# Performance work log

Hardware: AMD Instinct MI355X
Metric: run time of the kernel (lower is better)

Reference implementation:

```python
import jax, jax.numpy as jnp
import numpy as np
from jax import lax

B, T, DEPTH = 512, 32, 512
RNN, NCC = 512, 128
D_IN = DEPTH * (T * DEPTH // T // DEPTH) * 1 + NCC  # slice_len=1 -> 512 + 128 = 640


def setup_inputs() -> dict:
    key = jax.random.key(0)
    ks = jax.random.split(key, 7)
    s = 0.05  # tf.random_normal_initializer default stddev
    return {
        "f_pool": jax.random.normal(ks[0], (B, T, DEPTH), jnp.float32),
        "ground_truth": jax.random.normal(ks[1], (B, T, NCC), jnp.float32),
        "kernel": jax.random.normal(ks[2], (DEPTH + NCC, 4 * RNN), jnp.float32) * s,
        "rec_kernel": jax.random.normal(ks[3], (RNN, 4 * RNN), jnp.float32) * s,
        "bias": jax.random.normal(ks[4], (4 * RNN,), jnp.float32) * s,
        "softmax_w": jax.random.normal(ks[5], (RNN, NCC), jnp.float32) * s,
        "softmax_b": jax.random.normal(ks[6], (NCC,), jnp.float32) * s,
    }


def reference(f_pool, ground_truth, kernel, rec_kernel, bias, softmax_w, softmax_b):
    b, features_num, depth = f_pool.shape
    seq_length = ground_truth.shape[1]
    ncc = softmax_b.shape[0]
    rnn = rec_kernel.shape[0]
    slice_len = features_num // seq_length  # == 1 here
    gt_t = jnp.transpose(ground_truth, (1, 0, 2))  # [T, B, C] for scan

    def step(carry, inp):
        h, c, prev = carry
        t, gt_row = inp
        # image feature slice at char index t -> [B, slice_len*depth]
        feat = lax.dynamic_slice_in_dim(f_pool, t, slice_len, axis=1)
        feat = feat.reshape(b, slice_len * depth)
        x = jnp.concatenate([feat, prev], axis=1)
        z = x @ kernel + h @ rec_kernel + bias  # [B, 4*rnn]
        i, f, g, o = jnp.split(z, 4, axis=1)    # keras LSTMCell gate order
        c2 = jax.nn.sigmoid(f) * c + jax.nn.sigmoid(i) * jnp.tanh(g)
        h2 = jax.nn.sigmoid(o) * jnp.tanh(c2)
        logits = h2 @ softmax_w + softmax_b
        onehot = jax.nn.one_hot(jnp.argmax(logits, axis=1), ncc, dtype=f_pool.dtype)
        # teacher forcing: prev_output = ground_truth[:, t, :]
        return (h2, c2, gt_row), onehot

    h0 = jnp.zeros((b, rnn), f_pool.dtype)
    c0 = jnp.zeros((b, rnn), f_pool.dtype)
    prev0 = jnp.zeros((b, ncc), f_pool.dtype)
    (h, c, _), outs = lax.scan(step, (h0, c0, prev0), (jnp.arange(seq_length), gt_t))
    sequence_output = jnp.transpose(outs, (1, 0, 2))  # [B, T, C]
    return (sequence_output, h, c)
```

## Files before the change

kernel.cpp:

```cpp
#include <hip/hip_runtime.h>
#include <math.h>

typedef float  f32x4  __attribute__((ext_vector_type(4)));
typedef short  short8v __attribute__((ext_vector_type(8)));
typedef unsigned short ushort8v __attribute__((ext_vector_type(8)));
typedef unsigned short ushort4v __attribute__((ext_vector_type(4)));

#define KP_PRE 3840
#define KP_HS  1536

#define WAITV(N) asm volatile("s_waitcnt vmcnt(" #N ")" ::: "memory")
#define SBAR()   asm volatile("s_barrier" ::: "memory")

__device__ unsigned short g_Xb[16384][3840];
__device__ unsigned short g_Wb[2048][3840];
__device__ unsigned short g_Rb[2048][1536];
__device__ unsigned short g_hs[2][512][1536];
__device__ float g_pre[16384][2048];
__device__ float g_hf[2][512 * 512];
__device__ float g_swT[128][512];
__device__ float g_bperm[2048];
__device__ float g_plv[2][512 * 8];
__device__ int   g_pli[2][512 * 8];
__device__ unsigned g_xcnt[128];
__device__ unsigned g_xrel[128];

__global__ void init_counters()
{
    int t = threadIdx.x;
    if (t < 8) { g_xcnt[t * 16] = 0u; g_xrel[t * 16] = 0u; }
}

__device__ __forceinline__ unsigned short f2bf(float f) {
    unsigned u = __float_as_uint(f);
    return (unsigned short)((u + 0x7fffu + ((u >> 16) & 1u)) >> 16);
}
__device__ __forceinline__ float bf2f(unsigned short s) {
    return __uint_as_float(((unsigned)s) << 16);
}
__device__ __forceinline__ float sigf(float x) { return 1.f / (1.f + expf(-x)); }

__device__ __forceinline__ void split3(float v, unsigned short& s0,
                                       unsigned short& s1, unsigned short& s2) {
    s0 = f2bf(v); float f0 = bf2f(s0);
    s1 = f2bf(v - f0); float f1 = bf2f(s1);
    s2 = f2bf(v - f0 - f1);
}

__device__ __constant__ int c_ipt[6] = {0, 0, 1, 0, 1, 2};
__device__ __constant__ int c_jpt[6] = {0, 1, 0, 2, 1, 0};

__device__ __forceinline__ void gl16(const unsigned short* g, unsigned short* l) {
    __builtin_amdgcn_global_load_lds((const __attribute__((address_space(1))) void*)g,
                                     (__attribute__((address_space(3))) void*)l, 16, 0, 0);
}

__device__ __forceinline__ short8v fragld(const unsigned short* sh, int row, int uw) {
    return *(const short8v*)(sh + row * 64 + ((uw ^ (row & 7)) << 3));
}

template<int AUNITS, int BUNITS>
__device__ __forceinline__ void stage_chunk(const unsigned short* Ag, int pitchA,
                                            const unsigned short* Bg, int pitchB,
                                            int kb, unsigned short* slot, int tid)
{
#pragma unroll
    for (int v = 0; v < AUNITS / 256; ++v) {
        int e = v * 256 + tid;
        gl16(Ag + (size_t)(e >> 3) * pitchA + kb * 64 + (e & 7) * 8, slot + e * 8);
    }
#pragma unroll
    for (int v = 0; v < BUNITS / 256; ++v) {
        int e = v * 256 + tid;
        gl16(Bg + (size_t)(e >> 3) * pitchB + kb * 64 + (e & 7) * 8,
             slot + AUNITS * 8 + e * 8);
    }
}

__device__ __forceinline__ void stageA3(const unsigned short* Ag, int kr,
                                        unsigned short* buf, int tid)
{
#pragma unroll
    for (int s = 0; s < 3; ++s)
#pragma unroll
        for (int v = 0; v < 2; ++v) {
            int e = v * 256 + tid;
            gl16(Ag + (size_t)(e >> 3) * KP_HS + (s * 8 + kr) * 64 + (e & 7) * 8,
                 buf + s * 4096 + e * 8);
        }
}
__device__ __forceinline__ void stageB3(const unsigned short* Bg, int kr,
                                        unsigned short* buf, int tid)
{
#pragma unroll
    for (int s = 0; s < 3; ++s)
#pragma unroll
        for (int v = 0; v < 2; ++v) {
            int e = v * 256 + tid;
            gl16(Bg + (size_t)(e >> 3) * KP_HS + (s * 8 + kr) * 64 + (e & 7) * 8,
                 buf + 12288 + s * 4096 + e * 8);
        }
}
__device__ __forceinline__ void stage6(const unsigned short* Ag,
                                       const unsigned short* Bg,
                                       int kr, unsigned short* buf, int tid)
{
    stageA3(Ag, kr, buf, tid);
    stageB3(Bg, kr, buf, tid);
}

__global__ __launch_bounds__(256) void build_Xb(const float* __restrict__ fp,
                                                const float* __restrict__ gt)
{
    const int tid = threadIdx.x;
    const int m  = blockIdx.x * 16 + (tid >> 4);
    const int k8 = (blockIdx.y * 16 + (tid & 15)) * 8;
    const int t = m >> 9, b = m & 511;
    float x[8];
    if (k8 < 512) {
        float4 v0 = *(const float4*)(fp + ((size_t)(b * 32 + t)) * 512 + k8);
        float4 v1 = *(const float4*)(fp + ((size_t)(b * 32 + t)) * 512 + k8 + 4);
        x[0]=v0.x; x[1]=v0.y; x[2]=v0.z; x[3]=v0.w;
        x[4]=v1.x; x[5]=v1.y; x[6]=v1.z; x[7]=v1.w;
    } else if (t > 0) {
        float4 v0 = *(const float4*)(gt + ((size_t)(b * 32 + t - 1)) * 128 + (k8 - 512));
        float4 v1 = *(const float4*)(gt + ((size_t)(b * 32 + t - 1)) * 128 + (k8 - 512) + 4);
        x[0]=v0.x; x[1]=v0.y; x[2]=v0.z; x[3]=v0.w;
        x[4]=v1.x; x[5]=v1.y; x[6]=v1.z; x[7]=v1.w;
    } else {
#pragma unroll
        for (int j = 0; j < 8; ++j) x[j] = 0.f;
    }
    unsigned short s0[8], s1[8], s2[8];
#pragma unroll
    for (int j = 0; j < 8; ++j) split3(x[j], s0[j], s1[j], s2[j]);
    const int u = (k8 >> 3) & 7;
    const int base = (k8 & ~63) + (((u ^ (m & 7))) << 3);
#pragma unroll
    for (int p = 0; p < 6; ++p) {
        ushort8v v;
#pragma unroll
        for (int j = 0; j < 8; ++j)
            v[j] = (c_ipt[p] == 0) ? s0[j] : ((c_ipt[p] == 1) ? s1[j] : s2[j]);
        *(ushort8v*)&g_Xb[m][p * 640 + base] = v;
    }
}

__global__ __launch_bounds__(256) void build_Wb(const float* __restrict__ Wk)
{
    const int tid = threadIdx.x;
    const int np = blockIdx.x * 16 + (tid >> 4);
    const int k8 = (blockIdx.y * 16 + (tid & 15)) * 8;
    const int n = (np & 3) * 512 + (np >> 2);
    float x[8];
#pragma unroll
    for (int j = 0; j < 8; ++j) x[j] = Wk[(size_t)(k8 + j) * 2048 + n];
    unsigned short s0[8], s1[8], s2[8];
#pragma unroll
    for (int j = 0; j < 8; ++j) split3(x[j], s0[j], s1[j], s2[j]);
    const int u = (k8 >> 3) & 7;
    const int base = (k8 & ~63) + (((u ^ (np & 7))) << 3);
#pragma unroll
    for (int p = 0; p < 6; ++p) {
        ushort8v v;
#pragma unroll
        for (int j = 0; j < 8; ++j)
            v[j] = (c_jpt[p] == 0) ? s0[j] : ((c_jpt[p] == 1) ? s1[j] : s2[j]);
        *(ushort8v*)&g_Wb[np][p * 640 + base] = v;
    }
}

__global__ __launch_bounds__(256) void build_Rb(const float* __restrict__ Rk)
{
    const int tid = threadIdx.x;
    const int np = blockIdx.x * 16 + (tid >> 4);
    const int k8 = (blockIdx.y * 16 + (tid & 15)) * 8;
    const int n = (np & 3) * 512 + (np >> 2);
    float x[8];
#pragma unroll
    for (int j = 0; j < 8; ++j) x[j] = Rk[(size_t)(k8 + j) * 2048 + n];
    unsigned short s0[8], s1[8], s2[8];
#pragma unroll
    for (int j = 0; j < 8; ++j) split3(x[j], s0[j], s1[j], s2[j]);
    const int u = (k8 >> 3) & 7;
    const int base = (k8 & ~63) + (((u ^ (np & 7))) << 3);
    ushort8v v0, v1, v2;
#pragma unroll
    for (int j = 0; j < 8; ++j) { v0[j] = s0[j]; v1[j] = s1[j]; v2[j] = s2[j]; }
    *(ushort8v*)&g_Rb[np][0 * 512 + base] = v0;
    *(ushort8v*)&g_Rb[np][1 * 512 + base] = v1;
    *(ushort8v*)&g_Rb[np][2 * 512 + base] = v2;
}

__global__ __launch_bounds__(256) void build_misc(const float* __restrict__ sw,
                                                  const float* __restrict__ bias)
{
    int id = blockIdx.x * 256 + threadIdx.x;
    if (id < 128 * 512) {
        int c = id >> 9, r = id & 511;
        g_swT[c][r] = sw[(size_t)r * 128 + c];
    } else if (id < 128 * 512 + 2048) {
        int np = id - 128 * 512;
        g_bperm[np] = bias[(np & 3) * 512 + (np >> 2)];
    }
}

__global__ __launch_bounds__(256, 1) void pre_mfma()
{
    __shared__ __align__(16) char smem[98304];
    const int tid = threadIdx.x, lane = tid & 63, wave = tid >> 6;
    const int n0 = blockIdx.x * 64, m0 = blockIdx.y * 128;
    const int wr = wave >> 1, wc = wave & 1, l15 = lane & 15, ql = lane >> 4;
    unsigned short* ring = (unsigned short*)smem;
    const unsigned short* Ag = &g_Xb[m0][0];
    const unsigned short* Bg = &g_Wb[n0][0];

    f32x4 acc[4][2];
#pragma unroll
    for (int a = 0; a < 4; ++a)
#pragma unroll
        for (int b = 0; b < 2; ++b) acc[a][b] = (f32x4){0.f, 0.f, 0.f, 0.f};

    stage_chunk<1024, 512>(Ag, KP_PRE, Bg, KP_PRE, 0, ring + 0 * 12288, tid);
    stage_chunk<1024, 512>(Ag, KP_PRE, Bg, KP_PRE, 1, ring + 1 * 12288, tid);
    stage_chunk<1024, 512>(Ag, KP_PRE, Bg, KP_PRE, 2, ring + 2 * 12288, tid);
    for (int c = 0; c < 60; ++c) {
        if (c <= 57)      WAITV(12);
        else if (c == 58) WAITV(6);
        else              WAITV(0);
        SBAR();
        const unsigned short* Ac = ring + (c & 3) * 12288;
        const unsigned short* Bc = Ac + 8192;
#pragma unroll
        for (int sub = 0; sub < 2; ++sub) {
            const int uw = sub * 4 + ql;
            short8v af[4], bfr[2];
#pragma unroll
            for (int fa = 0; fa < 4; ++fa)
                af[fa] = fragld(Ac, wr * 64 + fa * 16 + l15, uw);
#pragma unroll
            for (int fb = 0; fb < 2; ++fb)
                bfr[fb] = fragld(Bc, wc * 32 + fb * 16 + l15, uw);
#pragma unroll
            for (int fa = 0; fa < 4; ++fa)
#pragma unroll
                for (int fb = 0; fb < 2; ++fb)
                    acc[fa][fb] = __builtin_amdgcn_mfma_f32_16x16x32_bf16(
                        af[fa], bfr[fb], acc[fa][fb], 0, 0, 0);
        }
        if (c + 3 < 60)
            stage_chunk<1024, 512>(Ag, KP_PRE, Bg, KP_PRE, c + 3,
                                   ring + ((c + 3) & 3) * 12288, tid);
    }
#pragma unroll
    for (int fa = 0; fa < 4; ++fa)
#pragma unroll
        for (int fb = 0; fb < 2; ++fb) {
            const int np = n0 + wc * 32 + fb * 16 + l15;
            const float bv = g_bperm[np];
#pragma unroll
            for (int q = 0; q < 4; ++q) {
                const int m = m0 + wr * 64 + fa * 16 + ql * 4 + q;
                g_pre[m][np] = acc[fa][fb][q] + bv;
            }
        }
}

__global__ __launch_bounds__(256, 1) void charnn_rec(
    const float* __restrict__ sb,
    float* __restrict__ seq, float* __restrict__ out_h, float* __restrict__ out_c)
{
    __shared__ __align__(16) char smem[147456];
    float (*zbuf)[68] = (float (*)[68])smem;
    unsigned short* ring = (unsigned short*)smem;

    const int bi = blockIdx.x, tid = threadIdx.x;
    const int lane = tid & 63, wave = tid >> 6;
    const int x  = bi & 7, jj = bi >> 3;
    const int Mg = x;
    const int Ng = jj;
    const int m0 = Mg * 64, n0 = Ng * 64;
    const int wr = wave >> 1, wc = wave & 1, l15 = lane & 15, ql = lane >> 4;

    const int m_e = tid >> 2;
    const int rb4 = (tid & 3) * 4;
    const int mg = m0 + m_e;
    float cst[4] = {0.f, 0.f, 0.f, 0.f};

    const int rgrp = Mg * 4 + (jj & 3);
    const int cg   = jj >> 2;
    const int arow = Mg * 64 + jj * 2;
    const bool xleader = (jj == 0);

    constexpr int ipt[6] = {0, 0, 1, 0, 1, 2};
    constexpr int jpt[6] = {0, 1, 0, 2, 1, 0};

    const unsigned short* Bg = &g_Rb[n0][0];

    f32x4 pq0, pq1, pq2, pq3;
    {
        const float* prow = &g_pre[0 * 512 + mg][n0];
        pq0 = *(const f32x4*)(prow + rb4 * 4);
        pq1 = *(const f32x4*)(prow + rb4 * 4 + 4);
        pq2 = *(const f32x4*)(prow + rb4 * 4 + 8);
        pq3 = *(const f32x4*)(prow + rb4 * 4 + 12);
    }

    for (int ph = 0; ph < 34; ++ph) {
        const int t = ph;
        const bool do_z = (ph >= 1 && ph <= 31);

        const unsigned short* Ag = nullptr;
        if (do_z) {
            Ag = &g_hs[(t + 1) & 1][m0][0];
            stageA3(Ag, 0, ring + 0 * 24576, tid);
            stageA3(Ag, 1, ring + 1 * 24576, tid);
            stageA3(Ag, 2, ring + 2 * 24576, tid);
        }

        if (ph >= 1 && ph <= 32) {
            const int tl = ph - 1;
            const int row = rgrp * 16 + (tid >> 4);
            const int col = cg * 16 + (tid & 15);
            const float* hrow = &g_hf[tl & 1][(size_t)row * 512];
            const float* wcol = &g_swT[col][0];
            float s0 = sb[col], s1 = 0.f, s2 = 0.f, s3 = 0.f;
#pragma unroll 8
            for (int k = 0; k < 512; k += 4) {
                float4 hv = *(const float4*)(hrow + k);
                float4 wv = *(const float4*)(wcol + k);
                s0 = fmaf(hv.x, wv.x, s0); s1 = fmaf(hv.y, wv.y, s1);
                s2 = fmaf(hv.z, wv.z, s2); s3 = fmaf(hv.w, wv.w, s3);
            }
            float bv = (s0 + s1) + (s2 + s3); int bidx = col;
#pragma unroll
            for (int m = 1; m < 16; m <<= 1) {
                float ov = __shfl_xor(bv, m, 64);
                int   oi = __shfl_xor(bidx, m, 64);
                if (ov > bv || (ov == bv && oi < bidx)) { bv = ov; bidx = oi; }
            }
            if ((tid & 15) == 0) {
                g_plv[tl & 1][row * 8 + cg] = bv;
                g_pli[tl & 1][row * 8 + cg] = bidx;
            }
        }

        if (ph >= 2 && wave < 2) {
            const int t2 = ph - 2;
            const int row = arow + wave;
            float v; int idx;
            if (lane < 8) {
                v   = g_plv[t2 & 1][row * 8 + lane];
                idx = g_pli[t2 & 1][row * 8 + lane];
            } else { v = -INFINITY; idx = 0x7fffffff; }
#pragma unroll
            for (int m = 1; m < 8; m <<= 1) {
                float ov = __shfl_xor(v, m, 64);
                int   oi = __shfl_xor(idx, m, 64);
                if (ov > v || (ov == v && oi < idx)) { v = ov; idx = oi; }
            }
            int win = __shfl(idx, 0, 64);
            if (lane < 32) {
                int c4 = lane * 4;
                float4 o;
                o.x = (c4 + 0 == win) ? 1.f : 0.f;
                o.y = (c4 + 1 == win) ? 1.f : 0.f;
                o.z = (c4 + 2 == win) ? 1.f : 0.f;
                o.w = (c4 + 3 == win) ? 1.f : 0.f;
                *(float4*)(seq + ((size_t)row * 32 + t2) * 128 + c4) = o;
            }
        }

        if (ph <= 31) {
            if (do_z) {
                f32x4 acc[2][2];
#pragma unroll
                for (int a = 0; a < 2; ++a)
#pragma unroll
                    for (int b = 0; b < 2; ++b) acc[a][b] = (f32x4){0.f, 0.f, 0.f, 0.f};
#pragma unroll
                for (int kr = 0; kr < 8; ++kr) {
                    if (kr >= 1 && kr <= 5)
                        stage6(Ag, Bg, kr + 2, ring + ((kr + 2) % 3) * 24576, tid);
                    if      (kr == 0) WAITV(12);
                    else if (kr == 1) WAITV(18);
                    else if (kr == 2) WAITV(24);
                    else if (kr == 3) WAITV(24);
                    else if (kr == 4) WAITV(24);
                    else if (kr == 5) WAITV(24);
                    else if (kr == 6) WAITV(12);
                    else              WAITV(0);
                    SBAR();
                    const unsigned short* Ab = ring + (kr % 3) * 24576;
                    const unsigned short* Bb = Ab + 12288;
#pragma unroll
                    for (int sub = 0; sub < 2; ++sub) {
                        const int uw = sub * 4 + ql;
                        short8v a0[2], a1[2], a2[2], b0[2], b1[2], b2[2];
                        a0[0] = fragld(Ab + 0 * 4096, wr * 32 + l15, uw);
                        a0[1] = fragld(Ab + 0 * 4096, wr * 32 + 16 + l15, uw);
                        a1[0] = fragld(Ab + 1 * 4096, wr * 32 + l15, uw);
                        a1[1] = fragld(Ab + 1 * 4096, wr * 32 + 16 + l15, uw);
                        a2[0] = fragld(Ab + 2 * 4096, wr * 32 + l15, uw);
                        a2[1] = fragld(Ab + 2 * 4096, wr * 32 + 16 + l15, uw);
                        b0[0] = fragld(Bb + 0 * 4096, wc * 32 + l15, uw);
                        b0[1] = fragld(Bb + 0 * 4096, wc * 32 + 16 + l15, uw);
                        b1[0] = fragld(Bb + 1 * 4096, wc * 32 + l15, uw);
                        b1[1] = fragld(Bb + 1 * 4096, wc * 32 + 16 + l15, uw);
                        b2[0] = fragld(Bb + 2 * 4096, wc * 32 + l15, uw);
                        b2[1] = fragld(Bb + 2 * 4096, wc * 32 + 16 + l15, uw);
#pragma unroll
                        for (int p = 0; p < 6; ++p) {
                            const short8v* A2 = (ipt[p] == 0) ? a0 :
                                                ((ipt[p] == 1) ? a1 : a2);
                            const short8v* B2 = (jpt[p] == 0) ? b0 :
                                                ((jpt[p] == 1) ? b1 : b2);
                            acc[0][0] = __builtin_amdgcn_mfma_f32_16x16x32_bf16(
                                A2[0], B2[0], acc[0][0], 0, 0, 0);
                            acc[0][1] = __builtin_amdgcn_mfma_f32_16x16x32_bf16(
                                A2[0], B2[1], acc[0][1], 0, 0, 0);
                            acc[1][0] = __builtin_amdgcn_mfma_f32_16x16x32_bf16(
                                A2[1], B2[0], acc[1][0], 0, 0, 0);
                            acc[1][1] = __builtin_amdgcn_mfma_f32_16x16x32_bf16(
                                A2[1], B2[1], acc[1][1], 0, 0, 0);
                        }
                    }
                }
                __syncthreads();
#pragma unroll
                for (int fa = 0; fa < 2; ++fa)
#pragma unroll
                    for (int fb = 0; fb < 2; ++fb)
#pragma unroll
                        for (int q2 = 0; q2 < 4; ++q2)
                            zbuf[wr * 32 + fa * 16 + ql * 4 + q2]
                                [wc * 32 + fb * 16 + l15] = acc[fa][fb][q2];
            }
            __syncthreads();

            unsigned short hs0[4], hs1[4], hs2[4];
            float hv4[4];
#pragma unroll
            for (int i = 0; i < 4; ++i) {
                const int rl = rb4 + i;
                float zi, zf, zg, zo;
                if (t > 0) {
                    float4 zq = *(const float4*)&zbuf[m_e][rl * 4];
                    zi = zq.x; zf = zq.y; zg = zq.z; zo = zq.w;
                } else { zi = zf = zg = zo = 0.f; }
                f32x4 pq = (i == 0) ? pq0 : ((i == 1) ? pq1 : ((i == 2) ? pq2 : pq3));
                zi += pq[0]; zf += pq[1]; zg += pq[2]; zo += pq[3];
                float c2 = sigf(zf) * cst[i] + sigf(zi) * tanhf(zg);
                float h2 = sigf(zo) * tanhf(c2);
                cst[i] = c2;
                hv4[i] = h2;
                split3(h2, hs0[i], hs1[i], hs2[i]);
            }
            const int r0g = Ng * 16 + rb4;
            *(float4*)&g_hf[t & 1][(size_t)mg * 512 + r0g] =
                make_float4(hv4[0], hv4[1], hv4[2], hv4[3]);
            if (t == 31) {
                *(float4*)&out_h[(size_t)mg * 512 + r0g] =
                    make_float4(hv4[0], hv4[1], hv4[2], hv4[3]);
                *(float4*)&out_c[(size_t)mg * 512 + r0g] =
                    make_float4(cst[0], cst[1], cst[2], cst[3]);
            }
            const int su = ((r0g >> 3) & 7) ^ (mg & 7);
            const int abase = (r0g & ~63) + (su << 3) + (r0g & 7);
#pragma unroll
            for (int i = 0; i < 3; ++i) {
                ushort4v v;
#pragma unroll
                for (int j = 0; j < 4; ++j)
                    v[j] = (i == 0) ? hs0[j] : ((i == 1) ? hs1[j] : hs2[j]);
                *(ushort4v*)&g_hs[t & 1][mg][i * 512 + abase] = v;
            }
        }

        if (ph < 33) {
            __syncthreads();

            if (ph <= 30) {
                stageB3(Bg, 0, ring + 0 * 24576, tid);
                stageB3(Bg, 1, ring + 1 * 24576, tid);
                stageB3(Bg, 2, ring + 2 * 24576, tid);
                const float* prow = &g_pre[(ph + 1) * 512 + mg][n0];
                pq0 = *(const f32x4*)(prow + rb4 * 4);
                pq1 = *(const f32x4*)(prow + rb4 * 4 + 4);
                pq2 = *(const f32x4*)(prow + rb4 * 4 + 8);
                pq3 = *(const f32x4*)(prow + rb4 * 4 + 12);
            }

            if (tid == 0) {
                __hip_atomic_fetch_add(&g_xcnt[x * 16], 1u,
                                       __ATOMIC_RELAXED, __HIP_MEMORY_SCOPE_AGENT);
                if (xleader) {
                    const unsigned xt = 32u * (unsigned)(ph + 1);
                    while (__hip_atomic_load(&g_xcnt[x * 16], __ATOMIC_RELAXED,
                                             __HIP_MEMORY_SCOPE_AGENT) < xt)
                        __builtin_amdgcn_s_sleep(2);
                    __hip_atomic_store(&g_xrel[x * 16], (unsigned)(ph + 1),
                                       __ATOMIC_RELAXED, __HIP_MEMORY_SCOPE_AGENT);
                }
                while (__hip_atomic_load(&g_xrel[x * 16], __ATOMIC_RELAXED,
                                         __HIP_MEMORY_SCOPE_AGENT) < (unsigned)(ph + 1))
                    __builtin_amdgcn_s_sleep(2);
                __builtin_amdgcn_fence(__ATOMIC_ACQUIRE, "agent");
            }
            __syncthreads();
        }
    }
}

extern "C" void kernel_launch(void* const* d_in, const int* in_sizes, int n_in,
                              void* d_out, int out_size, void* d_ws, size_t ws_size,
                              hipStream_t stream)
{
    const float* fp   = (const float*)d_in[0];
    const float* gt   = (const float*)d_in[1];
    const float* Wk   = (const float*)d_in[2];
    const float* Rk   = (const float*)d_in[3];
    const float* bias = (const float*)d_in[4];
    const float* sw   = (const float*)d_in[5];
    const float* sb   = (const float*)d_in[6];
    float* seq   = (float*)d_out;
    float* out_h = seq + (size_t)512 * 32 * 128;
    float* out_c = out_h + (size_t)512 * 512;

    hipLaunchKernelGGL(init_counters, dim3(1), dim3(64), 0, stream);
    hipLaunchKernelGGL(build_Xb, dim3(1024, 5), dim3(256), 0, stream, fp, gt);
    hipLaunchKernelGGL(build_Wb, dim3(128, 5), dim3(256), 0, stream, Wk);
    hipLaunchKernelGGL(build_Rb, dim3(128, 4), dim3(256), 0, stream, Rk);
    hipLaunchKernelGGL(build_misc, dim3(264), dim3(256), 0, stream, sw, bias);
    hipLaunchKernelGGL(pre_mfma, dim3(32, 128), dim3(256), 0, stream);
    hipLaunchKernelGGL(charnn_rec, dim3(256), dim3(256), 0, stream,
                       sb, seq, out_h, out_c);
}
```

Measured before the change: 1.711 ms.

## Double recurrent kernel block to 512 threads, halving per-wave MFMA and gate work

The persistent recurrent LSTM kernel now launches 512 threads per block instead of 256. Each of 8 waves computes a 32x16 output tile instead of 32x32, each thread handles two gate rows instead of four, and each thread issues half as many staging loads, with the vmcnt waits adjusted to match. The aim is to shorten the serial per-step critical path by spreading MFMA, LDS fragment loads and the gate epilogue over more waves. In exchange, the A fragments are loaded twice as often across waves and the block-wide barriers cost more with more waves.

```diff
diff --git a/kernel.cpp b/kernel.cpp
--- a/kernel.cpp
+++ b/kernel.cpp
@@ -4,7 +4,7 @@
 typedef float  f32x4  __attribute__((ext_vector_type(4)));
 typedef short  short8v __attribute__((ext_vector_type(8)));
 typedef unsigned short ushort8v __attribute__((ext_vector_type(8)));
-typedef unsigned short ushort4v __attribute__((ext_vector_type(4)));
+typedef unsigned short ushort2v __attribute__((ext_vector_type(2)));
 
 #define KP_PRE 3840
 #define KP_HS  1536
@@ -77,36 +77,32 @@
     }
 }
 
-__device__ __forceinline__ void stageA3(const unsigned short* Ag, int kr,
-                                        unsigned short* buf, int tid)
-{
-#pragma unroll
-    for (int s = 0; s < 3; ++s)
-#pragma unroll
-        for (int v = 0; v < 2; ++v) {
-            int e = v * 256 + tid;
-            gl16(Ag + (size_t)(e >> 3) * KP_HS + (s * 8 + kr) * 64 + (e & 7) * 8,
-                 buf + s * 4096 + e * 8);
-        }
-}
-__device__ __forceinline__ void stageB3(const unsigned short* Bg, int kr,
-                                        unsigned short* buf, int tid)
-{
-#pragma unroll
-    for (int s = 0; s < 3; ++s)
-#pragma unroll
-        for (int v = 0; v < 2; ++v) {
-            int e = v * 256 + tid;
-            gl16(Bg + (size_t)(e >> 3) * KP_HS + (s * 8 + kr) * 64 + (e & 7) * 8,
-                 buf + 12288 + s * 4096 + e * 8);
-        }
-}
-__device__ __forceinline__ void stage6(const unsigned short* Ag,
-                                       const unsigned short* Bg,
-                                       int kr, unsigned short* buf, int tid)
-{
-    stageA3(Ag, kr, buf, tid);
-    stageB3(Bg, kr, buf, tid);
+__device__ __forceinline__ void stageA3w(const unsigned short* Ag, int kr,
+                                         unsigned short* buf, int tid)
+{
+#pragma unroll
+    for (int s = 0; s < 3; ++s) {
+        int e = tid;
+        gl16(Ag + (size_t)(e >> 3) * KP_HS + (s * 8 + kr) * 64 + (e & 7) * 8,
+             buf + s * 4096 + e * 8);
+    }
+}
+__device__ __forceinline__ void stageB3w(const unsigned short* Bg, int kr,
+                                         unsigned short* buf, int tid)
+{
+#pragma unroll
+    for (int s = 0; s < 3; ++s) {
+        int e = tid;
+        gl16(Bg + (size_t)(e >> 3) * KP_HS + (s * 8 + kr) * 64 + (e & 7) * 8,
+             buf + 12288 + s * 4096 + e * 8);
+    }
+}
+__device__ __forceinline__ void stage6w(const unsigned short* Ag,
+                                        const unsigned short* Bg,
+                                        int kr, unsigned short* buf, int tid)
+{
+    stageA3w(Ag, kr, buf, tid);
+    stageB3w(Bg, kr, buf, tid);
 }
 
 __global__ __launch_bounds__(256) void build_Xb(const float* __restrict__ fp,
@@ -266,7 +262,7 @@
         }
 }
 
-__global__ __launch_bounds__(256, 1) void charnn_rec(
+__global__ __launch_bounds__(512, 1) void charnn_rec(
     const float* __restrict__ sb,
     float* __restrict__ seq, float* __restrict__ out_h, float* __restrict__ out_c)
 {
@@ -280,12 +276,12 @@
     const int Mg = x;
     const int Ng = jj;
     const int m0 = Mg * 64, n0 = Ng * 64;
-    const int wr = wave >> 1, wc = wave & 1, l15 = lane & 15, ql = lane >> 4;
-
-    const int m_e = tid >> 2;
-    const int rb4 = (tid & 3) * 4;
+    const int wr = wave >> 2, wc = wave & 3, l15 = lane & 15, ql = lane >> 4;
+
+    const int m_e = tid >> 3;
+    const int rb2 = (tid & 7) * 2;
     const int mg = m0 + m_e;
-    float cst[4] = {0.f, 0.f, 0.f, 0.f};
+    float cst[2] = {0.f, 0.f};
 
     const int rgrp = Mg * 4 + (jj & 3);
     const int cg   = jj >> 2;
@@ -297,13 +293,11 @@
 
     const unsigned short* Bg = &g_Rb[n0][0];
 
-    f32x4 pq0, pq1, pq2, pq3;
+    f32x4 pqa, pqb;
     {
         const float* prow = &g_pre[0 * 512 + mg][n0];
-        pq0 = *(const f32x4*)(prow + rb4 * 4);
-        pq1 = *(const f32x4*)(prow + rb4 * 4 + 4);
-        pq2 = *(const f32x4*)(prow + rb4 * 4 + 8);
-        pq3 = *(const f32x4*)(prow + rb4 * 4 + 12);
+        pqa = *(const f32x4*)(prow + rb2 * 4);
+        pqb = *(const f32x4*)(prow + rb2 * 4 + 4);
     }
 
     for (int ph = 0; ph < 34; ++ph) {
@@ -313,12 +307,12 @@
         const unsigned short* Ag = nullptr;
         if (do_z) {
             Ag = &g_hs[(t + 1) & 1][m0][0];
-            stageA3(Ag, 0, ring + 0 * 24576, tid);
-            stageA3(Ag, 1, ring + 1 * 24576, tid);
-            stageA3(Ag, 2, ring + 2 * 24576, tid);
-        }
-
-        if (ph >= 1 && ph <= 32) {
+            stageA3w(Ag, 0, ring + 0 * 24576, tid);
+            stageA3w(Ag, 1, ring + 1 * 24576, tid);
+            stageA3w(Ag, 2, ring + 2 * 24576, tid);
+        }
+
+        if (ph >= 1 && ph <= 32 && tid < 256) {
             const int tl = ph - 1;
             const int row = rgrp * 16 + (tid >> 4);
             const int col = cg * 16 + (tid & 15);
@@ -373,56 +367,44 @@
 
         if (ph <= 31) {
             if (do_z) {
-                f32x4 acc[2][2];
-#pragma unroll
-                for (int a = 0; a < 2; ++a)
-#pragma unroll
-                    for (int b = 0; b < 2; ++b) acc[a][b] = (f32x4){0.f, 0.f, 0.f, 0.f};
+                f32x4 acc[2];
+                acc[0] = (f32x4){0.f, 0.f, 0.f, 0.f};
+                acc[1] = (f32x4){0.f, 0.f, 0.f, 0.f};
 #pragma unroll
                 for (int kr = 0; kr < 8; ++kr) {
                     if (kr >= 1 && kr <= 5)
-                        stage6(Ag, Bg, kr + 2, ring + ((kr + 2) % 3) * 24576, tid);
-                    if      (kr == 0) WAITV(12);
-                    else if (kr == 1) WAITV(18);
-                    else if (kr == 2) WAITV(24);
-                    else if (kr == 3) WAITV(24);
-                    else if (kr == 4) WAITV(24);
-                    else if (kr == 5) WAITV(24);
-                    else if (kr == 6) WAITV(12);
-                    else              WAITV(0);
+                        stage6w(Ag, Bg, kr + 2, ring + ((kr + 2) % 3) * 24576, tid);
+                    if      (kr == 0) WAITV(6);
+                    else if (kr == 1) WAITV(9);
+                    else if (kr == 6) WAITV(6);
+                    else if (kr == 7) WAITV(0);
+                    else              WAITV(12);
                     SBAR();
                     const unsigned short* Ab = ring + (kr % 3) * 24576;
                     const unsigned short* Bb = Ab + 12288;
 #pragma unroll
                     for (int sub = 0; sub < 2; ++sub) {
                         const int uw = sub * 4 + ql;
-                        short8v a0[2], a1[2], a2[2], b0[2], b1[2], b2[2];
+                        short8v a0[2], a1[2], a2[2], b0, b1, b2;
                         a0[0] = fragld(Ab + 0 * 4096, wr * 32 + l15, uw);
                         a0[1] = fragld(Ab + 0 * 4096, wr * 32 + 16 + l15, uw);
                         a1[0] = fragld(Ab + 1 * 4096, wr * 32 + l15, uw);
                         a1[1] = fragld(Ab + 1 * 4096, wr * 32 + 16 + l15, uw);
                         a2[0] = fragld(Ab + 2 * 4096, wr * 32 + l15, uw);
                         a2[1] = fragld(Ab + 2 * 4096, wr * 32 + 16 + l15, uw);
-                        b0[0] = fragld(Bb + 0 * 4096, wc * 32 + l15, uw);
-                        b0[1] = fragld(Bb + 0 * 4096, wc * 32 + 16 + l15, uw);
-                        b1[0] = fragld(Bb + 1 * 4096, wc * 32 + l15, uw);
-                        b1[1] = fragld(Bb + 1 * 4096, wc * 32 + 16 + l15, uw);
-                        b2[0] = fragld(Bb + 2 * 4096, wc * 32 + l15, uw);
-                        b2[1] = fragld(Bb + 2 * 4096, wc * 32 + 16 + l15, uw);
+                        b0 = fragld(Bb + 0 * 4096, wc * 16 + l15, uw);
+                        b1 = fragld(Bb + 1 * 4096, wc * 16 + l15, uw);
+                        b2 = fragld(Bb + 2 * 4096, wc * 16 + l15, uw);
 #pragma unroll
                         for (int p = 0; p < 6; ++p) {
                             const short8v* A2 = (ipt[p] == 0) ? a0 :
                                                 ((ipt[p] == 1) ? a1 : a2);
-                            const short8v* B2 = (jpt[p] == 0) ? b0 :
+                            const short8v  B2 = (jpt[p] == 0) ? b0 :
                                                 ((jpt[p] == 1) ? b1 : b2);
-                            acc[0][0] = __builtin_amdgcn_mfma_f32_16x16x32_bf16(
-                                A2[0], B2[0], acc[0][0], 0, 0, 0);
-                            acc[0][1] = __builtin_amdgcn_mfma_f32_16x16x32_bf16(
-                                A2[0], B2[1], acc[0][1], 0, 0, 0);
-                            acc[1][0] = __builtin_amdgcn_mfma_f32_16x16x32_bf16(
-                                A2[1], B2[0], acc[1][0], 0, 0, 0);
-                            acc[1][1] = __builtin_amdgcn_mfma_f32_16x16x32_bf16(
-                                A2[1], B2[1], acc[1][1], 0, 0, 0);
+                            acc[0] = __builtin_amdgcn_mfma_f32_16x16x32_bf16(
+                                A2[0], B2, acc[0], 0, 0, 0);
+                            acc[1] = __builtin_amdgcn_mfma_f32_16x16x32_bf16(
+                                A2[1], B2, acc[1], 0, 0, 0);
                         }
                     }
                 }
@@ -430,50 +412,48 @@
 #pragma unroll
                 for (int fa = 0; fa < 2; ++fa)
 #pragma unroll
-                    for (int fb = 0; fb < 2; ++fb)
-#pragma unroll
-                        for (int q2 = 0; q2 < 4; ++q2)
-                            zbuf[wr * 32 + fa * 16 + ql * 4 + q2]
-                                [wc * 32 + fb * 16 + l15] = acc[fa][fb][q2];
+                    for (int q2 = 0; q2 < 4; ++q2)
+                        zbuf[wr * 32 + fa * 16 + ql * 4 + q2]
+                            [wc * 16 + l15] = acc[fa][q2];
             }
             __syncthreads();
 
-            unsigned short hs0[4], hs1[4], hs2[4];
-            float hv4[4];
-#pragma unroll
-            for (int i = 0; i < 4; ++i) {
-                const int rl = rb4 + i;
+            unsigned short hs0[2], hs1[2], hs2[2];
+            float hv2[2];
+#pragma unroll
+            for (int i = 0; i < 2; ++i) {
+                const int rl = rb2 + i;
                 float zi, zf, zg, zo;
                 if (t > 0) {
                     float4 zq = *(const float4*)&zbuf[m_e][rl * 4];
                     zi = zq.x; zf = zq.y; zg = zq.z; zo = zq.w;
                 } else { zi = zf = zg = zo = 0.f; }
-                f32x4 pq = (i == 0) ? pq0 : ((i == 1) ? pq1 : ((i == 2) ? pq2 : pq3));
+                f32x4 pq = (i == 0) ? pqa : pqb;
                 zi += pq[0]; zf += pq[1]; zg += pq[2]; zo += pq[3];
                 float c2 = sigf(zf) * cst[i] + sigf(zi) * tanhf(zg);
                 float h2 = sigf(zo) * tanhf(c2);
                 cst[i] = c2;
-                hv4[i] = h2;
+                hv2[i] = h2;
                 split3(h2, hs0[i], hs1[i], hs2[i]);
             }
-            const int r0g = Ng * 16 + rb4;
-            *(float4*)&g_hf[t & 1][(size_t)mg * 512 + r0g] =
-                make_float4(hv4[0], hv4[1], hv4[2], hv4[3]);
+            const int r0g = Ng * 16 + rb2;
+            *(float2*)&g_hf[t & 1][(size_t)mg * 512 + r0g] =
+                make_float2(hv2[0], hv2[1]);
             if (t == 31) {
-                *(float4*)&out_h[(size_t)mg * 512 + r0g] =
-                    make_float4(hv4[0], hv4[1], hv4[2], hv4[3]);
-                *(float4*)&out_c[(size_t)mg * 512 + r0g] =
-                    make_float4(cst[0], cst[1], cst[2], cst[3]);
+                *(float2*)&out_h[(size_t)mg * 512 + r0g] =
+                    make_float2(hv2[0], hv2[1]);
+                *(float2*)&out_c[(size_t)mg * 512 + r0g] =
+                    make_float2(cst[0], cst[1]);
             }
             const int su = ((r0g >> 3) & 7) ^ (mg & 7);
             const int abase = (r0g & ~63) + (su << 3) + (r0g & 7);
 #pragma unroll
             for (int i = 0; i < 3; ++i) {
-                ushort4v v;
-#pragma unroll
-                for (int j = 0; j < 4; ++j)
+                ushort2v v;
+#pragma unroll
+                for (int j = 0; j < 2; ++j)
                     v[j] = (i == 0) ? hs0[j] : ((i == 1) ? hs1[j] : hs2[j]);
-                *(ushort4v*)&g_hs[t & 1][mg][i * 512 + abase] = v;
+                *(ushort2v*)&g_hs[t & 1][mg][i * 512 + abase] = v;
             }
         }
 
@@ -481,14 +461,12 @@
             __syncthreads();
 
             if (ph <= 30) {
-                stageB3(Bg, 0, ring + 0 * 24576, tid);
-                stageB3(Bg, 1, ring + 1 * 24576, tid);
-                stageB3(Bg, 2, ring + 2 * 24576, tid);
+                stageB3w(Bg, 0, ring + 0 * 24576, tid);
+                stageB3w(Bg, 1, ring + 1 * 24576, tid);
+                stageB3w(Bg, 2, ring + 2 * 24576, tid);
                 const float* prow = &g_pre[(ph + 1) * 512 + mg][n0];
-                pq0 = *(const f32x4*)(prow + rb4 * 4);
-                pq1 = *(const f32x4*)(prow + rb4 * 4 + 4);
-                pq2 = *(const f32x4*)(prow + rb4 * 4 + 8);
-                pq3 = *(const f32x4*)(prow + rb4 * 4 + 12);
+                pqa = *(const f32x4*)(prow + rb2 * 4);
+                pqb = *(const f32x4*)(prow + rb2 * 4 + 4);
             }
 
             if (tid == 0) {
@@ -533,6 +511,6 @@
     hipLaunchKernelGGL(build_Rb, dim3(128, 4), dim3(256), 0, stream, Rk);
     hipLaunchKernelGGL(build_misc, dim3(264), dim3(256), 0, stream, sw, bias);
     hipLaunchKernelGGL(pre_mfma, dim3(32, 128), dim3(256), 0, stream);
-    hipLaunchKernelGGL(charnn_rec, dim3(256), dim3(256), 0, stream,
+    hipLaunchKernelGGL(charnn_rec, dim3(256), dim3(512), 0, stream,
                        sb, seq, out_h, out_c);
 }
```

Result: faster. 1.643 ms (-4.0%).
